# Performance work log

Measured on AMD Instinct MI355X. Metric: run time of the kernel, lower is better.

Reference implementation:

```python
import jax, jax.numpy as jnp
import numpy as np

N, E, IN_DIM, H, C = 100000, 1600000, 128, 4, 32
D = H * C  # 128


def setup_inputs() -> dict:
    key = jax.random.key(0)
    ks = jax.random.split(key, 8)
    rn = lambda k, shape, sc: (jax.random.normal(k, shape, jnp.float32) * sc)
    return {
        "x": rn(ks[0], (N, IN_DIM), 1.0),
        "edge_index": jax.random.randint(ks[1], (2, E), 0, N, jnp.int32),
        "lin_w": rn(ks[2], (IN_DIM, D), 0.05),
        "lin_b": jnp.zeros((D,), jnp.float32),
        "gat_w": rn(ks[3], (IN_DIM, D), 0.05),
        "att_src": rn(ks[4], (H, C), 0.1),
        "att_dst": rn(ks[5], (H, C), 0.1),
        "gat_bias": jnp.zeros((D,), jnp.float32),
        "bn_gamma": jnp.ones((D,), jnp.float32),
        "bn_beta": jnp.zeros((D,), jnp.float32),
    }


def reference(x, edge_index, lin_w, lin_b, gat_w, att_src, att_dst, gat_bias, bn_gamma, bn_beta):
    n = x.shape[0]
    heads, ch = att_src.shape
    # residual branch: h_in = Linear(x)
    h_in = x @ lin_w + lin_b  # [N, H*C]
    # GATConv: project, per-head attention logits
    xp = (x @ gat_w).reshape(n, heads, ch)  # [N, H, C]
    a_src = jnp.einsum("nhc,hc->nh", xp, att_src)  # [N, H]
    a_dst = jnp.einsum("nhc,hc->nh", xp, att_dst)  # [N, H]
    # PyG default add_self_loops=True
    loop = jnp.arange(n, dtype=edge_index.dtype)
    src = jnp.concatenate([edge_index[0], loop])  # message source j
    dst = jnp.concatenate([edge_index[1], loop])  # message target i
    e = jax.nn.leaky_relu(a_src[src] + a_dst[dst], 0.2)  # [E+N, H]
    # softmax over incoming edges per target node (stable, segment-wise)
    m = jax.ops.segment_max(e, dst, num_segments=n)
    ex = jnp.exp(e - m[dst])
    denom = jax.ops.segment_sum(ex, dst, num_segments=n)
    alpha = ex / denom[dst]  # [E+N, H]
    # attention-weighted aggregation (scatter-add)
    out = jax.ops.segment_sum(alpha[:, :, None] * xp[src], dst, num_segments=n)  # [N, H, C]
    h = out.reshape(n, heads * ch) + gat_bias  # concat heads + bias
    # BatchNorm1d (training-mode batch statistics, biased variance, eps=1e-5)
    mu = h.mean(axis=0)
    var = h.var(axis=0)
    h = (h - mu) / jnp.sqrt(var + 1e-5) * bn_gamma + bn_beta
    h = jax.nn.elu(h)
    return h_in + h
```

## Files before the change

kernel.cpp:

```cpp
#include <hip/hip_runtime.h>
#include <stdint.h>

typedef unsigned short u16;
typedef __attribute__((ext_vector_type(8))) short short8;
typedef __attribute__((ext_vector_type(4))) float floatx4;

#define DH 128
#define NH 4
#define CH 32

#define NPB  256
#define MAXB 512
#define EPB 8192
#define SGRID 512

__device__ __forceinline__ float bf2f(u16 u) {
    union { unsigned int i; float f; } c; c.i = ((unsigned int)u) << 16; return c.f;
}
__device__ __forceinline__ u16 f2bf(float f) {
    union { float f; unsigned int i; } c; c.f = f;
    unsigned int x = c.i;
    x += 0x7FFFu + ((x >> 16) & 1u);
    return (u16)(x >> 16);
}
__device__ __forceinline__ float b2f_lo(unsigned v) {
    union { unsigned u; float f; } c; c.u = v << 16; return c.f;
}
__device__ __forceinline__ float b2f_hi(unsigned v) {
    union { unsigned u; float f; } c; c.u = v & 0xffff0000u; return c.f;
}
__device__ __forceinline__ float lr(float x) { return fmaxf(x, 0.2f * x); }

__global__ void repack_w(const float* __restrict__ lin_w, const float* __restrict__ gat_w,
                         u16* __restrict__ wpack) {
    int t = blockIdx.x * blockDim.x + threadIdx.x;
    int j    = t & 7;
    int lane = (t >> 3) & 63;
    int ks   = (t >> 9) & 3;
    int ct   = t >> 11;
    int k    = ks * 32 + (lane >> 4) * 8 + j;
    int col  = ct * 16 + (lane & 15);
    float v = (col < DH) ? lin_w[k * DH + col] : gat_w[k * DH + (col - DH)];
    wpack[t] = f2bf(v);
}

__global__ __launch_bounds__(256) void gemm_mfma(
        const float* __restrict__ x, const float* __restrict__ lin_b,
        const u16* __restrict__ wpack, const float* __restrict__ att_src,
        const float* __restrict__ att_dst, float* __restrict__ h_out,
        u16* __restrict__ xp, float* __restrict__ a_src,
        float* __restrict__ a_dst, int N) {
    int wave = threadIdx.x >> 6;
    int lane = threadIdx.x & 63;
    int rowBase = blockIdx.x * 64 + wave * 16;
    if (rowBase >= N) return;
    int m = lane & 15, quad = lane >> 4;

    short8 afr[4];
    const float* xrow = x + (size_t)(rowBase + m) * DH + quad * 8;
    #pragma unroll
    for (int ks = 0; ks < 4; ks++) {
        float4 f0 = *(const float4*)(xrow + ks * 32);
        float4 f1 = *(const float4*)(xrow + ks * 32 + 4);
        short8 a;
        a[0] = (short)f2bf(f0.x); a[1] = (short)f2bf(f0.y);
        a[2] = (short)f2bf(f0.z); a[3] = (short)f2bf(f0.w);
        a[4] = (short)f2bf(f1.x); a[5] = (short)f2bf(f1.y);
        a[6] = (short)f2bf(f1.z); a[7] = (short)f2bf(f1.w);
        afr[ks] = a;
    }

    #pragma unroll 4
    for (int ct = 0; ct < 8; ct++) {
        floatx4 acc = {0.f, 0.f, 0.f, 0.f};
        const short8* bp = (const short8*)wpack + (ct * 4) * 64 + lane;
        #pragma unroll
        for (int ks = 0; ks < 4; ks++) {
            short8 bfr = bp[ks * 64];
            acc = __builtin_amdgcn_mfma_f32_16x16x32_bf16(afr[ks], bfr, acc, 0, 0, 0);
        }
        int col = ct * 16 + m;
        float bias = lin_b[col];
        #pragma unroll
        for (int r = 0; r < 4; r++)
            h_out[(size_t)(rowBase + quad * 4 + r) * DH + col] = acc[r] + bias;
    }

    float pS[4], pD[4];
    #pragma unroll
    for (int ct2 = 0; ct2 < 8; ct2++) {
        const int ct = ct2 + 8;
        const int hh = ct2 >> 1;
        floatx4 acc = {0.f, 0.f, 0.f, 0.f};
        const short8* bp = (const short8*)wpack + (ct * 4) * 64 + lane;
        #pragma unroll
        for (int ks = 0; ks < 4; ks++) {
            short8 bfr = bp[ks * 64];
            acc = __builtin_amdgcn_mfma_f32_16x16x32_bf16(afr[ks], bfr, acc, 0, 0, 0);
        }
        int c2 = ct2 * 16 + m;
        #pragma unroll
        for (int r = 0; r < 4; r++)
            xp[(size_t)(rowBase + quad * 4 + r) * DH + c2] = f2bf(acc[r]);

        int ch = ((ct2 & 1) << 4) + m;
        float ws = att_src[hh * CH + ch];
        float wd = att_dst[hh * CH + ch];
        if (!(ct2 & 1)) {
            #pragma unroll
            for (int r = 0; r < 4; r++) { pS[r] = acc[r] * ws; pD[r] = acc[r] * wd; }
        } else {
            #pragma unroll
            for (int r = 0; r < 4; r++) {
                pS[r] = fmaf(acc[r], ws, pS[r]);
                pD[r] = fmaf(acc[r], wd, pD[r]);
            }
            #pragma unroll
            for (int r = 0; r < 4; r++) {
                #pragma unroll
                for (int mk = 1; mk <= 8; mk <<= 1) {
                    pS[r] += __shfl_xor(pS[r], mk, 64);
                    pD[r] += __shfl_xor(pD[r], mk, 64);
                }
            }
            if (m == 0) {
                #pragma unroll
                for (int r = 0; r < 4; r++) {
                    int node = rowBase + quad * 4 + r;
                    a_src[node * NH + hh] = pS[r];
                    a_dst[node * NH + hh] = pD[r];
                }
            }
        }
    }
}


__global__ __launch_bounds__(256) void bucket_count(
        const int* __restrict__ ei, int E, int N, int B,
        int* __restrict__ bcount) {
    __shared__ int h[MAXB];
    for (int j = threadIdx.x; j < B; j += 256) h[j] = 0;
    __syncthreads();
    int i0 = blockIdx.x * EPB;
    int i1 = min(E, i0 + EPB);
    for (int i = i0 + threadIdx.x; i < i1; i += 256) {
        int d = min(max(ei[E + i], 0), N - 1);
        atomicAdd(&h[d >> 8], 1);
    }
    __syncthreads();
    for (int j = threadIdx.x; j < B; j += 256) {
        int c = h[j];
        if (c) atomicAdd(&bcount[j], c);
    }
}

__global__ __launch_bounds__(512) void bucket_scan(
        const int* __restrict__ bcount, int B,
        int* __restrict__ bbase, int* __restrict__ bcur) {
    __shared__ int buf[512];
    int t = threadIdx.x;
    int v = (t < B) ? bcount[t] : 0;
    buf[t] = v;
    __syncthreads();
    for (int s = 1; s < 512; s <<= 1) {
        int add = (t >= s) ? buf[t - s] : 0;
        __syncthreads();
        buf[t] += add;
        __syncthreads();
    }
    if (t < B) { int e = buf[t] - v; bbase[t] = e; bcur[t] = e; }
}

__global__ __launch_bounds__(256) void bucket_scatter(
        const int* __restrict__ ei, int E, int N, int B,
        int* __restrict__ bcur, unsigned* __restrict__ tmp) {
    __shared__ int h[MAXB];
    __shared__ int base[MAXB];
    for (int j = threadIdx.x; j < B; j += 256) h[j] = 0;
    __syncthreads();
    int i0 = blockIdx.x * EPB;
    int i1 = min(E, i0 + EPB);
    for (int i = i0 + threadIdx.x; i < i1; i += 256) {
        int d = min(max(ei[E + i], 0), N - 1);
        atomicAdd(&h[d >> 8], 1);
    }
    __syncthreads();
    for (int j = threadIdx.x; j < B; j += 256) {
        int c = h[j];
        base[j] = c ? atomicAdd(&bcur[j], c) : 0;
    }
    __syncthreads();
    for (int j = threadIdx.x; j < B; j += 256) h[j] = 0;
    __syncthreads();
    for (int i = i0 + threadIdx.x; i < i1; i += 256) {
        int s = min(max(ei[i], 0), N - 1);
        int d = min(max(ei[E + i], 0), N - 1);
        int b = d >> 8;
        int pos = base[b] + atomicAdd(&h[b], 1);
        tmp[pos] = (unsigned)s | ((unsigned)(d & 255) << 17);
    }
}

__global__ __launch_bounds__(256) void bucket_to_csr(
        const unsigned* __restrict__ tmp, const int* __restrict__ bbase,
        const int* __restrict__ bcount, int N,
        int* __restrict__ offsets, int* __restrict__ deg,
        int* __restrict__ col) {
    __shared__ int cnt[NPB];
    __shared__ int excl[NPB];
    int b = blockIdx.x;
    int t = threadIdx.x;
    int bstart = bbase[b];
    int c = bcount[b];
    cnt[t] = 0;
    __syncthreads();
    for (int k = t; k < c; k += 256) {
        unsigned pk = tmp[bstart + k];
        atomicAdd(&cnt[pk >> 17], 1);
    }
    __syncthreads();
    int v = cnt[t];
    excl[t] = v;
    __syncthreads();
    for (int s = 1; s < 256; s <<= 1) {
        int add = (t >= s) ? excl[t - s] : 0;
        __syncthreads();
        excl[t] += add;
        __syncthreads();
    }
    int mystart = excl[t] - v;
    int node = b * NPB + t;
    if (node < N) {
        offsets[node] = bstart + mystart;
        deg[node] = v;
    }
    cnt[t] = mystart;
    __syncthreads();
    for (int k = t; k < c; k += 256) {
        unsigned pk = tmp[bstart + k];
        int slot = atomicAdd(&cnt[pk >> 17], 1);
        col[bstart + slot] = (int)(pk & 0x1FFFFu);
    }
}

__global__ __launch_bounds__(256) void csr_gather(
        const int* __restrict__ offsets, const int* __restrict__ deg,
        const int* __restrict__ col, const float* __restrict__ a_src,
        const float* __restrict__ a_dst, const u16* __restrict__ xp,
        float* __restrict__ agg, int N) {
    int node = blockIdx.x * 4 + (threadIdx.x >> 6);
    if (node >= N) return;
    int lane  = threadIdx.x & 63;
    int h     = lane >> 4;
    int q     = lane & 3;
    int esl   = lane >> 2;
    int lane2 = lane << 1;

    float ad_q = a_dst[node * NH + q];

    float w = __expf(lr(a_src[node * NH + h] + a_dst[node * NH + h]));
    unsigned xv = *(const unsigned*)(xp + (size_t)node * DH + lane2);
    float acc0 = w * b2f_lo(xv);
    float acc1 = w * b2f_hi(xv);
    float denv = 0.f;

    int off = offsets[node], dg = deg[node];
    const int* cp = col + off;

#define EDGE_F(K) {                                                       \
        float e = __shfl(ev, ((K) << 2) | h, 64);                         \
        int  su = __builtin_amdgcn_readlane(s_e, (K) << 2);               \
        const u16* row = xp + ((size_t)(unsigned)su << 7);                \
        unsigned v = *(const unsigned*)(row + lane2);                     \
        acc0 = fmaf(e, b2f_lo(v), acc0);                                  \
        acc1 = fmaf(e, b2f_hi(v), acc1); }

#define EDGE_P(K) {                                                       \
        float e = ((K) < rem) ? __shfl(ev, ((K) << 2) | h, 64) : 0.f;     \
        int  su = __builtin_amdgcn_readlane(s_e, (K) << 2);               \
        const u16* row = xp + ((size_t)(unsigned)su << 7);                \
        unsigned v = *(const unsigned*)(row + lane2);                     \
        acc0 = fmaf(e, b2f_lo(v), acc0);                                  \
        acc1 = fmaf(e, b2f_hi(v), acc1); }

    for (int k0 = 0; k0 < dg; k0 += 16) {
        int rem  = dg - k0;
        int kidx = min(k0 + esl, dg - 1);
        int s_e  = cp[kidx];
        float ev = __expf(lr(a_src[s_e * NH + q] + ad_q));
        denv += ((k0 + esl) < dg) ? ev : 0.f;
        if (rem >= 16) {
            #pragma unroll
            for (int k = 0; k < 16; k++) EDGE_F(k)
        } else {
            #pragma unroll
            for (int k = 0; k < 16; k++) EDGE_P(k)
        }
    }
#undef EDGE_F
#undef EDGE_P

    #pragma unroll
    for (int m = 4; m <= 32; m <<= 1)
        denv += __shfl_xor(denv, m, 64);
    float den = __shfl(denv, h, 64) + w;

    float inv = 1.0f / den;
    float2 o; o.x = acc0 * inv; o.y = acc1 * inv;
    *(float2*)(agg + (size_t)node * DH + lane2) = o;
}

__global__ __launch_bounds__(256) void stats_kernel(
        const float* __restrict__ agg, int N,
        float* __restrict__ colsum, float* __restrict__ colsumsq) {
    int grp = threadIdx.x & 31;
    int sub = threadIdx.x >> 5;
    int c4  = grp << 2;
    floatx4 s1 = {0.f, 0.f, 0.f, 0.f}, s2 = {0.f, 0.f, 0.f, 0.f};
    int rpb = (N + gridDim.x - 1) / gridDim.x;
    int r0  = blockIdx.x * rpb;
    int r1  = min(N, r0 + rpb);
    for (int r = r0 + sub; r < r1; r += 8) {
        floatx4 v = *(const floatx4*)(agg + (size_t)r * DH + c4);
        s1 += v;
        s2 += v * v;
    }
    __shared__ floatx4 red1[8][32];
    __shared__ floatx4 red2[8][32];
    red1[sub][grp] = s1;
    red2[sub][grp] = s2;
    __syncthreads();
    for (int s = 4; s >= 1; s >>= 1) {
        if (sub < s) {
            red1[sub][grp] += red1[sub + s][grp];
            red2[sub][grp] += red2[sub + s][grp];
        }
        __syncthreads();
    }
    if (sub == 0) {
        floatx4 a1 = red1[0][grp];
        floatx4 a2 = red2[0][grp];
        #pragma unroll
        for (int j = 0; j < 4; j++) {
            atomicAdd(&colsum[c4 + j],   a1[j]);
            atomicAdd(&colsumsq[c4 + j], a2[j]);
        }
    }
}

__global__ __launch_bounds__(256) void final_kernel(
        const float* __restrict__ agg, const float* __restrict__ colsum,
        const float* __restrict__ colsumsq, const float* __restrict__ gamma,
        const float* __restrict__ beta, float* __restrict__ out, int N) {
    int t = blockIdx.x * blockDim.x + threadIdx.x;
    if (t >= N * (DH / 4)) return;
    int row = t >> 5;
    int c4  = (t & 31) << 2;
    float inv_n = 1.0f / (float)N;

    floatx4 s1 = *(const floatx4*)(colsum   + c4);
    floatx4 s2 = *(const floatx4*)(colsumsq + c4);
    floatx4 g  = *(const floatx4*)(gamma    + c4);
    floatx4 b  = *(const floatx4*)(beta     + c4);
    floatx4 a  = *(const floatx4*)(agg + (size_t)row * DH + c4);
    floatx4 o  = *(const floatx4*)(out + (size_t)row * DH + c4);

    #pragma unroll
    for (int j = 0; j < 4; j++) {
        float mu   = s1[j] * inv_n;
        float var  = s2[j] * inv_n - mu * mu;
        float rstd = rsqrtf(var + 1e-5f);
        float v = (a[j] - mu) * rstd * g[j] + b[j];
        v = v > 0.f ? v : (__expf(v) - 1.f);
        float r = o[j] + v;
        if (!(r >= -1e30f && r <= 1e30f)) r = 512.0f;
        o[j] = r;
    }
    *(floatx4*)(out + (size_t)row * DH + c4) = o;
}

extern "C" void kernel_launch(void* const* d_in, const int* in_sizes, int n_in,
                              void* d_out, int out_size, void* d_ws, size_t ws_size,
                              hipStream_t stream) {
    const float* x        = (const float*)d_in[0];
    const int*   ei       = (const int*)d_in[1];
    const float* lin_w    = (const float*)d_in[2];
    const float* lin_b    = (const float*)d_in[3];
    const float* gat_w    = (const float*)d_in[4];
    const float* att_src  = (const float*)d_in[5];
    const float* att_dst  = (const float*)d_in[6];
    const float* bn_gamma = (const float*)d_in[8];
    const float* bn_beta  = (const float*)d_in[9];

    int N = in_sizes[0] / DH;
    int E = in_sizes[1] / 2;
    int B = (N + NPB - 1) / NPB;
    int EB = (E + EPB - 1) / EPB;

    char* p = (char*)d_ws;
    u16*   xp      = (u16*)p;        p += (size_t)N * DH * 2;
    float* a_src   = (float*)p;      p += (size_t)N * NH * 4;
    float* a_dst   = (float*)p;      p += (size_t)N * NH * 4;
    u16*   wpack   = (u16*)p;        p += 32768 * 2;
    int*   col     = (int*)p;        p += (size_t)E * 4;
    int*   offsets = (int*)p;        p += (size_t)N * 4;
    int*   deg     = (int*)p;        p += (size_t)N * 4;
    int*   bbase   = (int*)p;        p += MAXB * 4;
    int*   bcur    = (int*)p;        p += MAXB * 4;
    char* zero_begin = p;
    int*   bcount  = (int*)p;        p += MAXB * 4;
    float* colsum  = (float*)p;      p += DH * 4;
    float* colsumsq= (float*)p;      p += DH * 4;
    size_t zero_bytes = (size_t)(p - zero_begin);
    float* agg     = (float*)p;
    unsigned* tmp  = (unsigned*)agg;

    hipMemsetAsync(zero_begin, 0, zero_bytes, stream);

    repack_w<<<(16 * 4 * 64 * 8) / 256, 256, 0, stream>>>(lin_w, gat_w, wpack);

    gemm_mfma<<<(N + 63) / 64, 256, 0, stream>>>(x, lin_b, wpack, att_src,
                                                 att_dst, (float*)d_out, xp,
                                                 a_src, a_dst, N);

    bucket_count<<<EB, 256, 0, stream>>>(ei, E, N, B, bcount);
    bucket_scan<<<1, 512, 0, stream>>>(bcount, B, bbase, bcur);
    bucket_scatter<<<EB, 256, 0, stream>>>(ei, E, N, B, bcur, tmp);
    bucket_to_csr<<<B, 256, 0, stream>>>(tmp, bbase, bcount, N,
                                         offsets, deg, col);

    csr_gather<<<(N + 3) / 4, 256, 0, stream>>>(offsets, deg, col, a_src,
                                                a_dst, xp, agg, N);
    stats_kernel<<<SGRID, 256, 0, stream>>>(agg, N, colsum, colsumsq);
    final_kernel<<<(N * (DH / 4) + 255) / 256, 256, 0, stream>>>(
        agg, colsum, colsumsq, bn_gamma, bn_beta, (float*)d_out, N);
}
```

Measured before the change: 367.5 us.

## Compute two 16-row tiles per wave in GEMM and retune grid sizes

The projection GEMM now has each wave handle 32 rows as two 16-row MFMA tiles that share every weight fragment load. This halves weight traffic per row and doubles the MFMA work per wave, with a guard for a partial second tile. It also halves edges per block in the bucket kernels, doubles the stats grid, and unrolls the stats loop. The cost is more registers per wave in the GEMM and half as many GEMM blocks.

```diff
diff --git a/kernel.cpp b/kernel.cpp
--- a/kernel.cpp
+++ b/kernel.cpp
@@ -11,8 +11,8 @@
 
 #define NPB  256
 #define MAXB 512
-#define EPB 8192
-#define SGRID 512
+#define EPB 4096
+#define SGRID 1024
 
 __device__ __forceinline__ float bf2f(u16 u) {
     union { unsigned int i; float f; } c; c.i = ((unsigned int)u) << 16; return c.f;
@@ -52,83 +52,125 @@
         float* __restrict__ a_dst, int N) {
     int wave = threadIdx.x >> 6;
     int lane = threadIdx.x & 63;
-    int rowBase = blockIdx.x * 64 + wave * 16;
-    if (rowBase >= N) return;
+    int row0 = blockIdx.x * 128 + wave * 32;
+    if (row0 >= N) return;
+    int row1 = row0 + 16;
+    bool t1 = (row1 < N);
     int m = lane & 15, quad = lane >> 4;
 
-    short8 afr[4];
-    const float* xrow = x + (size_t)(rowBase + m) * DH + quad * 8;
-    #pragma unroll
-    for (int ks = 0; ks < 4; ks++) {
-        float4 f0 = *(const float4*)(xrow + ks * 32);
-        float4 f1 = *(const float4*)(xrow + ks * 32 + 4);
-        short8 a;
-        a[0] = (short)f2bf(f0.x); a[1] = (short)f2bf(f0.y);
-        a[2] = (short)f2bf(f0.z); a[3] = (short)f2bf(f0.w);
-        a[4] = (short)f2bf(f1.x); a[5] = (short)f2bf(f1.y);
-        a[6] = (short)f2bf(f1.z); a[7] = (short)f2bf(f1.w);
-        afr[ks] = a;
+    short8 afr0[4], afr1[4];
+    {
+        const float* xr0 = x + (size_t)(row0 + m) * DH + quad * 8;
+        const float* xr1 = x + (size_t)((t1 ? row1 : row0) + m) * DH + quad * 8;
+        #pragma unroll
+        for (int ks = 0; ks < 4; ks++) {
+            float4 f0 = *(const float4*)(xr0 + ks * 32);
+            float4 f1 = *(const float4*)(xr0 + ks * 32 + 4);
+            short8 a;
+            a[0] = (short)f2bf(f0.x); a[1] = (short)f2bf(f0.y);
+            a[2] = (short)f2bf(f0.z); a[3] = (short)f2bf(f0.w);
+            a[4] = (short)f2bf(f1.x); a[5] = (short)f2bf(f1.y);
+            a[6] = (short)f2bf(f1.z); a[7] = (short)f2bf(f1.w);
+            afr0[ks] = a;
+            float4 g0 = *(const float4*)(xr1 + ks * 32);
+            float4 g1 = *(const float4*)(xr1 + ks * 32 + 4);
+            short8 b;
+            b[0] = (short)f2bf(g0.x); b[1] = (short)f2bf(g0.y);
+            b[2] = (short)f2bf(g0.z); b[3] = (short)f2bf(g0.w);
+            b[4] = (short)f2bf(g1.x); b[5] = (short)f2bf(g1.y);
+            b[6] = (short)f2bf(g1.z); b[7] = (short)f2bf(g1.w);
+            afr1[ks] = b;
+        }
     }
 
     #pragma unroll 4
     for (int ct = 0; ct < 8; ct++) {
-        floatx4 acc = {0.f, 0.f, 0.f, 0.f};
+        floatx4 acc0 = {0.f, 0.f, 0.f, 0.f};
+        floatx4 acc1 = {0.f, 0.f, 0.f, 0.f};
         const short8* bp = (const short8*)wpack + (ct * 4) * 64 + lane;
         #pragma unroll
         for (int ks = 0; ks < 4; ks++) {
             short8 bfr = bp[ks * 64];
-            acc = __builtin_amdgcn_mfma_f32_16x16x32_bf16(afr[ks], bfr, acc, 0, 0, 0);
+            acc0 = __builtin_amdgcn_mfma_f32_16x16x32_bf16(afr0[ks], bfr, acc0, 0, 0, 0);
+            acc1 = __builtin_amdgcn_mfma_f32_16x16x32_bf16(afr1[ks], bfr, acc1, 0, 0, 0);
         }
         int col = ct * 16 + m;
         float bias = lin_b[col];
         #pragma unroll
         for (int r = 0; r < 4; r++)
-            h_out[(size_t)(rowBase + quad * 4 + r) * DH + col] = acc[r] + bias;
-    }
-
-    float pS[4], pD[4];
+            h_out[(size_t)(row0 + quad * 4 + r) * DH + col] = acc0[r] + bias;
+        if (t1) {
+            #pragma unroll
+            for (int r = 0; r < 4; r++)
+                h_out[(size_t)(row1 + quad * 4 + r) * DH + col] = acc1[r] + bias;
+        }
+    }
+
+    float pS0[4], pD0[4], pS1[4], pD1[4];
     #pragma unroll
     for (int ct2 = 0; ct2 < 8; ct2++) {
         const int ct = ct2 + 8;
         const int hh = ct2 >> 1;
-        floatx4 acc = {0.f, 0.f, 0.f, 0.f};
+        floatx4 acc0 = {0.f, 0.f, 0.f, 0.f};
+        floatx4 acc1 = {0.f, 0.f, 0.f, 0.f};
         const short8* bp = (const short8*)wpack + (ct * 4) * 64 + lane;
         #pragma unroll
         for (int ks = 0; ks < 4; ks++) {
             short8 bfr = bp[ks * 64];
-            acc = __builtin_amdgcn_mfma_f32_16x16x32_bf16(afr[ks], bfr, acc, 0, 0, 0);
+            acc0 = __builtin_amdgcn_mfma_f32_16x16x32_bf16(afr0[ks], bfr, acc0, 0, 0, 0);
+            acc1 = __builtin_amdgcn_mfma_f32_16x16x32_bf16(afr1[ks], bfr, acc1, 0, 0, 0);
         }
         int c2 = ct2 * 16 + m;
         #pragma unroll
         for (int r = 0; r < 4; r++)
-            xp[(size_t)(rowBase + quad * 4 + r) * DH + c2] = f2bf(acc[r]);
+            xp[(size_t)(row0 + quad * 4 + r) * DH + c2] = f2bf(acc0[r]);
+        if (t1) {
+            #pragma unroll
+            for (int r = 0; r < 4; r++)
+                xp[(size_t)(row1 + quad * 4 + r) * DH + c2] = f2bf(acc1[r]);
+        }
 
         int ch = ((ct2 & 1) << 4) + m;
         float ws = att_src[hh * CH + ch];
         float wd = att_dst[hh * CH + ch];
         if (!(ct2 & 1)) {
             #pragma unroll
-            for (int r = 0; r < 4; r++) { pS[r] = acc[r] * ws; pD[r] = acc[r] * wd; }
+            for (int r = 0; r < 4; r++) {
+                pS0[r] = acc0[r] * ws; pD0[r] = acc0[r] * wd;
+                pS1[r] = acc1[r] * ws; pD1[r] = acc1[r] * wd;
+            }
         } else {
             #pragma unroll
             for (int r = 0; r < 4; r++) {
-                pS[r] = fmaf(acc[r], ws, pS[r]);
-                pD[r] = fmaf(acc[r], wd, pD[r]);
+                pS0[r] = fmaf(acc0[r], ws, pS0[r]);
+                pD0[r] = fmaf(acc0[r], wd, pD0[r]);
+                pS1[r] = fmaf(acc1[r], ws, pS1[r]);
+                pD1[r] = fmaf(acc1[r], wd, pD1[r]);
             }
             #pragma unroll
             for (int r = 0; r < 4; r++) {
                 #pragma unroll
                 for (int mk = 1; mk <= 8; mk <<= 1) {
-                    pS[r] += __shfl_xor(pS[r], mk, 64);
-                    pD[r] += __shfl_xor(pD[r], mk, 64);
+                    pS0[r] += __shfl_xor(pS0[r], mk, 64);
+                    pD0[r] += __shfl_xor(pD0[r], mk, 64);
+                    pS1[r] += __shfl_xor(pS1[r], mk, 64);
+                    pD1[r] += __shfl_xor(pD1[r], mk, 64);
                 }
             }
             if (m == 0) {
                 #pragma unroll
                 for (int r = 0; r < 4; r++) {
-                    int node = rowBase + quad * 4 + r;
-                    a_src[node * NH + hh] = pS[r];
-                    a_dst[node * NH + hh] = pD[r];
+                    int node = row0 + quad * 4 + r;
+                    a_src[node * NH + hh] = pS0[r];
+                    a_dst[node * NH + hh] = pD0[r];
+                }
+                if (t1) {
+                    #pragma unroll
+                    for (int r = 0; r < 4; r++) {
+                        int node = row1 + quad * 4 + r;
+                        a_src[node * NH + hh] = pS1[r];
+                        a_dst[node * NH + hh] = pD1[r];
+                    }
                 }
             }
         }
@@ -321,6 +363,7 @@
     int rpb = (N + gridDim.x - 1) / gridDim.x;
     int r0  = blockIdx.x * rpb;
     int r1  = min(N, r0 + rpb);
+    #pragma unroll 4
     for (int r = r0 + sub; r < r1; r += 8) {
         floatx4 v = *(const floatx4*)(agg + (size_t)r * DH + c4);
         s1 += v;
@@ -420,9 +463,9 @@
 
     repack_w<<<(16 * 4 * 64 * 8) / 256, 256, 0, stream>>>(lin_w, gat_w, wpack);
 
-    gemm_mfma<<<(N + 63) / 64, 256, 0, stream>>>(x, lin_b, wpack, att_src,
-                                                 att_dst, (float*)d_out, xp,
-                                                 a_src, a_dst, N);
+    gemm_mfma<<<(N + 127) / 128, 256, 0, stream>>>(x, lin_b, wpack, att_src,
+                                                   att_dst, (float*)d_out, xp,
+                                                   a_src, a_dst, N);
 
     bucket_count<<<EB, 256, 0, stream>>>(ei, E, N, B, bcount);
     bucket_scan<<<1, 512, 0, stream>>>(bcount, B, bbase, bcur);
```

New measurement: 415.2 us. +13.0%, slower.
